# Optimization experiments

Measured on AMD Instinct MI355X. Metric: run time of the kernel, lower is better.

## Reference

```python
import jax, jax.numpy as jnp
import numpy as np

DIM_MODEL = 512
DIM_HEAD = 64


def setup_inputs() -> dict:
    key = jax.random.key(0)
    ks = jax.random.split(key, 7)
    B, S = 4, 4096
    x = jax.random.normal(ks[0], (B, S, DIM_MODEL), dtype=jnp.float32)
    mask = jnp.ones((B, 1, S), dtype=jnp.int32)
    # torch Linear init: U(-1/sqrt(fan_in), 1/sqrt(fan_in)); stored as (in, out) for x @ W
    bound = 1.0 / np.sqrt(DIM_MODEL)
    Wq = jax.random.uniform(ks[1], (DIM_MODEL, DIM_HEAD), minval=-bound, maxval=bound, dtype=jnp.float32)
    bq = jax.random.uniform(ks[2], (DIM_HEAD,), minval=-bound, maxval=bound, dtype=jnp.float32)
    Wk = jax.random.uniform(ks[3], (DIM_MODEL, DIM_HEAD), minval=-bound, maxval=bound, dtype=jnp.float32)
    bk = jax.random.uniform(ks[4], (DIM_HEAD,), minval=-bound, maxval=bound, dtype=jnp.float32)
    Wv = jax.random.uniform(ks[5], (DIM_MODEL, DIM_HEAD), minval=-bound, maxval=bound, dtype=jnp.float32)
    bv = jax.random.uniform(ks[6], (DIM_HEAD,), minval=-bound, maxval=bound, dtype=jnp.float32)
    return {"x": x, "mask": mask, "Wq": Wq, "bq": bq, "Wk": Wk, "bk": bk, "Wv": Wv, "bv": bv}


def reference(x, mask, Wq, bq, Wk, bk, Wv, bv):
    # single-head QKV projection
    q = x @ Wq + bq  # (B, S, Dh)
    k = x @ Wk + bk
    v = x @ Wv + bv
    dot_scale = jnp.sqrt(jnp.float32(DIM_HEAD))
    # explicit O(S^2) score matrix, softmax over keys
    scores = jnp.einsum("bqd,bkd->bqk", q, k) / dot_scale  # (B, S, S)
    attn = jax.nn.softmax(scores, axis=-1)
    # faithful to source: mask applied AFTER softmax with -inf fill
    attn = jnp.where(mask == 0, jnp.float32(-jnp.inf), attn)
    return jnp.einsum("bqk,bkd->bqd", attn, v)  # (B, S, Dh)
```

## Files before the change

kernel.cpp:

```cpp
#include <hip/hip_runtime.h>
#include <hip/hip_bf16.h>

typedef _Float16 half8v __attribute__((ext_vector_type(8)));
typedef _Float16 half4v __attribute__((ext_vector_type(4)));
typedef _Float16 half2v __attribute__((ext_vector_type(2)));
typedef __fp16   fp16x2 __attribute__((ext_vector_type(2)));
typedef __attribute__((ext_vector_type(4))) float floatx4;

#define LOG2E_OVER_8 0.18033688011112042f

#if __has_builtin(__builtin_amdgcn_exp2f)
#define EXP2(x) __builtin_amdgcn_exp2f(x)
#else
#define EXP2(x) exp2f(x)
#endif


__device__ __forceinline__ void gload_lds16(const void* g, void* l) {
    __builtin_amdgcn_global_load_lds(
        (const __attribute__((address_space(1))) void*)(unsigned long long)g,
        (__attribute__((address_space(3))) void*)(unsigned)(unsigned long long)l,
        16, 0, 0);
}

__global__ __launch_bounds__(256) void wtrans_k(const float* __restrict__ Wq,
                                                const float* __restrict__ Wk,
                                                const float* __restrict__ Wv,
                                                _Float16* __restrict__ Wt) {
    int idx = blockIdx.x * 256 + threadIdx.x;
    int p = idx >> 15, rem = idx & 32767;
    int k = rem >> 6;
    int n = rem & 63;
    const float* W = (p == 0) ? Wq : ((p == 1) ? Wk : Wv);
    int ctg = p * 4 + (n >> 4), m = n & 15;
    int kc = k >> 5, quad = (k >> 3) & 3, j = k & 7;
    Wt[(((ctg << 4) + kc) * 64 + (quad << 4) + m) * 8 + j] = (_Float16)W[k * 64 + n];
}

#define XS_STRIDE 536
__global__ __launch_bounds__(256) void proj_k(const float* __restrict__ x,
                                              const _Float16* __restrict__ Wt,
                                              const float* __restrict__ bq,
                                              const float* __restrict__ bk,
                                              const float* __restrict__ bv,
                                              _Float16* __restrict__ Qh,
                                              _Float16* __restrict__ Kh,
                                              _Float16* __restrict__ Vh) {
    __shared__ _Float16 xs[2][16 * XS_STRIDE];

    int tid = threadIdx.x, l = tid & 63, wv = tid >> 6;
    int m = l & 15, quad = l >> 4;
    int row0 = blockIdx.x * 32;

#pragma unroll
    for (int s = 0; s < 2; s++)
#pragma unroll
        for (int i = 0; i < 8; i++) {
            int idx = tid + i * 256;
            int row = idx >> 7, c4 = idx & 127;
            float4 v = *(const float4*)(x + (row0 + s * 16 + row) * 512 + c4 * 4);
            union { half2v h[2]; uint2 u; } cv;
            cv.h[0][0] = (_Float16)v.x; cv.h[0][1] = (_Float16)v.y;
            cv.h[1][0] = (_Float16)v.z; cv.h[1][1] = (_Float16)v.w;
            *(uint2*)(xs[s] + row * XS_STRIDE + c4 * 4) = cv.u;
        }
    __syncthreads();

    const _Float16* arow0 = xs[0] + m * XS_STRIDE + quad * 8;
    const _Float16* arow1 = xs[1] + m * XS_STRIDE + quad * 8;

    floatx4 acc[2][3];
#pragma unroll
    for (int s = 0; s < 2; s++)
#pragma unroll
        for (int i = 0; i < 3; i++) acc[s][i] = (floatx4)(0.f);

#pragma unroll 4
    for (int kc = 0; kc < 16; kc++) {
        half8v a0 = *(const half8v*)(arow0 + kc * 32);
        half8v a1 = *(const half8v*)(arow1 + kc * 32);
#pragma unroll
        for (int ct = 0; ct < 3; ct++) {
            int ctg = wv * 3 + ct;
            half8v b = *(const half8v*)(Wt + (((ctg << 4) + kc) * 64 + l) * 8);
            acc[0][ct] = __builtin_amdgcn_mfma_f32_16x16x32_f16(a0, b, acc[0][ct], 0, 0, 0);
            acc[1][ct] = __builtin_amdgcn_mfma_f32_16x16x32_f16(a1, b, acc[1][ct], 0, 0, 0);
        }
    }

#pragma unroll
    for (int s = 0; s < 2; s++) {
        int rowb = row0 + s * 16;
#pragma unroll
        for (int ct = 0; ct < 3; ct++) {
            int ctg = wv * 3 + ct;
            int col = ctg * 16 + m;
            float bias = (ctg < 4) ? bq[col] : ((ctg < 8) ? bk[col - 64] : bv[col - 128]);
            if (ctg < 8) {
                _Float16* dst = (ctg < 4) ? Qh : Kh;
                float scl = (ctg < 4) ? LOG2E_OVER_8 : 1.0f;
                int dd = (ctg & 3) * 16 + m;
                int c = dd >> 5, quadQ = (dd >> 3) & 3, j = dd & 7;
#pragma unroll
                for (int r = 0; r < 4; r++) {
                    int row = rowb + quad * 4 + r;
                    int chunk = ((row >> 4) << 1) + c;
                    dst[(chunk * 64 + quadQ * 16 + (row & 15)) * 8 + j] =
                        (_Float16)((acc[s][ct][r] + bias) * scl);
                }
            } else {
                int dt = ctg - 8;
                int t64 = rowb >> 6, ktp = (rowb >> 5) & 1, half = (rowb >> 4) & 1;
                int chunk = t64 * 8 + dt * 2 + ktp;
                union { _Float16 h[4]; unsigned long long u; } pk;
#pragma unroll
                for (int r = 0; r < 4; r++) pk.h[r] = (_Float16)(acc[s][ct][r] + bias);
                *(unsigned long long*)(Vh + (chunk * 64 + quad * 16 + m) * 8 + half * 4) = pk.u;
            }
        }
    }
}

template <int NT>
__global__ __launch_bounds__(256, 4) void attn_k(const _Float16* __restrict__ Qh,
                                                 const _Float16* __restrict__ Kh,
                                                 const _Float16* __restrict__ Vh,
                                                 const int* __restrict__ mask,
                                                 _Float16* __restrict__ Np,
                                                 float* __restrict__ Dp,
                                                 int gshift) {
    __shared__ __align__(16) uint4 stage_lds[2][1024];

    int tid = threadIdx.x, l = tid & 63, wv = tid >> 6;
    int m = l & 15, quad = l >> 4;
    int bid = blockIdx.x;
    int grp = bid & ((1 << gshift) - 1), qblk = bid >> gshift;
    int os = grp >> 2, b = grp & 3;
    int q0 = qblk * 64 + wv * 16;

    const int* maskb = mask + b * 4096 + os * (NT * 64);
    int az = 0;
#pragma unroll
    for (int i = 0; i < NT; i++) az |= (maskb[l + i * 64] == 0);
    const bool hasz = __any(az);

    int qt_g = (b * 4096 + q0) >> 4;
    half8v qf[2];
#pragma unroll
    for (int c = 0; c < 2; c++)
        qf[c] = *(const half8v*)(Qh + ((qt_g * 2 + c) * 64 + l) * 8);

    half8v ones8;
#pragma unroll
    for (int i = 0; i < 8; i++) ones8[i] = (_Float16)1.0f;

    int tb0 = (b * 64 + os * NT) * 512;
    const uint4* kh4 = (const uint4*)Kh + tb0;
    const uint4* vh4 = (const uint4*)Vh + tb0;

    floatx4 oacc[4];
#pragma unroll
    for (int dt = 0; dt < 4; dt++) oacc[dt] = (floatx4)(0.f);
    floatx4 oden = (floatx4)(0.f);

#pragma unroll
    for (int i = 0; i < 2; i++) {
        int idx = wv * 128 + i * 64 + l;
        gload_lds16(kh4 + idx, &stage_lds[0][0] + idx);
        gload_lds16(vh4 + idx, &stage_lds[0][512] + idx);
    }
    __syncthreads();

    for (int t = 0; t < NT; t++) {
        int cur = t & 1;
        if (t + 1 < NT) {
            const uint4* ksrc = kh4 + (t + 1) * 512;
            const uint4* vsrc = vh4 + (t + 1) * 512;
            uint4* kb = &stage_lds[cur ^ 1][0];
            uint4* vb = &stage_lds[cur ^ 1][512];
#pragma unroll
            for (int i = 0; i < 2; i++) {
                int idx = wv * 128 + i * 64 + l;
                gload_lds16(ksrc + idx, kb + idx);
                gload_lds16(vsrc + idx, vb + idx);
            }
        }
        const uint4* kt4 = &stage_lds[cur][0];
        const uint4* vt4 = &stage_lds[cur][512];
#pragma unroll
        for (int sp = 0; sp < 2; sp++) {
            union { uint4 u; half8v h; } kk[4];
#pragma unroll
            for (int i = 0; i < 4; i++)
                kk[i].u = kt4[(sp * 4 + i) * 64 + l];
            uint4 vv[4];
#pragma unroll
            for (int dt = 0; dt < 4; dt++)
                vv[dt] = vt4[(dt * 2 + sp) * 64 + l];
            half8v pb8;
            {
                union { fp16x2 h2[4]; half8v h8; } pu;
#pragma unroll
                for (int se = 0; se < 2; se++) {
                    floatx4 sf = (floatx4)(0.f);
                    __builtin_amdgcn_s_setprio(1);
                    sf = __builtin_amdgcn_mfma_f32_16x16x32_f16(kk[se * 2 + 0].h, qf[0], sf, 0, 0, 0);
                    sf = __builtin_amdgcn_mfma_f32_16x16x32_f16(kk[se * 2 + 1].h, qf[1], sf, 0, 0, 0);
                    __builtin_amdgcn_s_setprio(0);
                    float p0 = EXP2(sf[0]), p1 = EXP2(sf[1]);
                    float p2 = EXP2(sf[2]), p3 = EXP2(sf[3]);
                    if (hasz) {
                        int kg = t * 64 + (sp * 2 + se) * 16 + quad * 4;
                        if (maskb[kg + 0] == 0) p0 = -__builtin_inff();
                        if (maskb[kg + 1] == 0) p1 = -__builtin_inff();
                        if (maskb[kg + 2] == 0) p2 = -__builtin_inff();
                        if (maskb[kg + 3] == 0) p3 = -__builtin_inff();
                    }
                    pu.h2[se * 2 + 0] = __builtin_amdgcn_cvt_pkrtz(p0, p1);
                    pu.h2[se * 2 + 1] = __builtin_amdgcn_cvt_pkrtz(p2, p3);
                }
                pb8 = pu.h8;
            }
            __builtin_amdgcn_s_setprio(1);
            oden = __builtin_amdgcn_mfma_f32_16x16x32_f16(ones8, pb8, oden, 0, 0, 0);
#pragma unroll
            for (int dt = 0; dt < 4; dt++) {
                union { uint4 u; half8v h; } vc; vc.u = vv[dt];
                oacc[dt] = __builtin_amdgcn_mfma_f32_16x16x32_f16(vc.h, pb8, oacc[dt], 0, 0, 0);
            }
            __builtin_amdgcn_s_setprio(0);
        }
        __syncthreads();
    }

    float* Tw = (float*)&stage_lds[0][0] + wv * (16 * 68);
    int rowb = os * 16384 + b * 4096 + q0;
    if (l < 16) Dp[rowb + l] = oden[0];
#pragma unroll
    for (int dt = 0; dt < 4; dt++)
#pragma unroll
        for (int r = 0; r < 4; r++)
            Tw[m * 68 + dt * 16 + quad * 4 + r] = oacc[dt][r];
    asm volatile("s_waitcnt lgkmcnt(0)" ::: "memory");
    __builtin_amdgcn_sched_barrier(0);
#pragma unroll
    for (int g = 0; g < 4; g++) {
        int idx = g * 64 + l;
        int row = idx >> 4, c4 = (idx & 15) * 4;
        float4 v = *(const float4*)(Tw + row * 68 + c4);
        union { half4v h; unsigned long long u; } pk;
        pk.h[0] = (_Float16)v.x; pk.h[1] = (_Float16)v.y;
        pk.h[2] = (_Float16)v.z; pk.h[3] = (_Float16)v.w;
        *(unsigned long long*)(Np + (size_t)(rowb + row) * 64 + c4) = pk.u;
    }
}

__global__ __launch_bounds__(256) void combine_k(const _Float16* __restrict__ Np,
                                                 const float* __restrict__ Dp,
                                                 float* __restrict__ out,
                                                 int spl) {
    int g4 = blockIdx.x * 256 + threadIdx.x;
    int row = g4 >> 4;
    float4 nu = make_float4(0.f, 0.f, 0.f, 0.f);
    float d = 0.f;
    for (int sp = 0; sp < spl; sp++) {
        union { unsigned long long u; half4v h; } v;
        v.u = *(const unsigned long long*)(Np + ((size_t)sp << 20) + (size_t)g4 * 4);
        nu.x += (float)v.h[0]; nu.y += (float)v.h[1];
        nu.z += (float)v.h[2]; nu.w += (float)v.h[3];
        d += Dp[sp * 16384 + row];
    }
    float inv = 1.0f / d;
    ((float4*)out)[g4] = make_float4(nu.x * inv, nu.y * inv, nu.z * inv, nu.w * inv);
}

extern "C" void kernel_launch(void* const* d_in, const int* in_sizes, int n_in,
                              void* d_out, int out_size, void* d_ws, size_t ws_size,
                              hipStream_t stream) {
    const float* x  = (const float*)d_in[0];
    const int* mask = (const int*)d_in[1];
    const float* Wq = (const float*)d_in[2];
    const float* bq = (const float*)d_in[3];
    const float* Wk = (const float*)d_in[4];
    const float* bk = (const float*)d_in[5];
    const float* Wv = (const float*)d_in[6];
    const float* bv = (const float*)d_in[7];
    float* out = (float*)d_out;

    char* ws = (char*)d_ws;
    _Float16* Wt = (_Float16*)(ws);
    _Float16* Qh = (_Float16*)(ws + 0x40000);
    _Float16* Kh = (_Float16*)(ws + 0x240000);
    _Float16* Vh = (_Float16*)(ws + 0x440000);
    float*    Dp = (float*)(ws + 0x640000);
    _Float16* Np = (_Float16*)(ws + 0x740000);

    wtrans_k<<<384, 256, 0, stream>>>(Wq, Wk, Wv, Wt);
    proj_k<<<512, 256, 0, stream>>>(x, Wt, bq, bk, bv, Qh, Kh, Vh);
    attn_k<16><<<64 * 16, 256, 0, stream>>>(Qh, Kh, Vh, mask, Np, Dp, 4);
    combine_k<<<1024, 256, 0, stream>>>(Np, Dp, out, 4);
}
```

Before: 123.0 us.

## Read K/V tiles directly from global memory and double the key-split count

Drops the double-buffered global-to-LDS staging of K/V tiles in the attention kernel, so each wave reads its K/V fragments straight from global memory (through the caches). This removes the per-tile block barriers. LDS is now used only for the output transpose, and launch bounds are raised to target more waves per SIMD. The key dimension is also split into 8 partitions instead of 4, doubling the grid and halving the tiles per block, with the combine kernel merging 8 partials. The risks are redundant global/L2 traffic, since the four waves of a block all load the same K/V data, more exposed load latency without prefetch, and extra partial output to combine.

Result: slower. 140.1 us (+13.9%).

```diff
diff --git a/kernel.cpp b/kernel.cpp
--- a/kernel.cpp
+++ b/kernel.cpp
@@ -15,13 +15,6 @@
 #define EXP2(x) exp2f(x)
 #endif
 
-
-__device__ __forceinline__ void gload_lds16(const void* g, void* l) {
-    __builtin_amdgcn_global_load_lds(
-        (const __attribute__((address_space(1))) void*)(unsigned long long)g,
-        (__attribute__((address_space(3))) void*)(unsigned)(unsigned long long)l,
-        16, 0, 0);
-}
 
 __global__ __launch_bounds__(256) void wtrans_k(const float* __restrict__ Wq,
                                                 const float* __restrict__ Wk,
@@ -122,14 +115,14 @@
 }
 
 template <int NT>
-__global__ __launch_bounds__(256, 4) void attn_k(const _Float16* __restrict__ Qh,
+__global__ __launch_bounds__(256, 6) void attn_k(const _Float16* __restrict__ Qh,
                                                  const _Float16* __restrict__ Kh,
                                                  const _Float16* __restrict__ Vh,
                                                  const int* __restrict__ mask,
                                                  _Float16* __restrict__ Np,
                                                  float* __restrict__ Dp,
                                                  int gshift) {
-    __shared__ __align__(16) uint4 stage_lds[2][1024];
+    __shared__ float T[4][16 * 68];
 
     int tid = threadIdx.x, l = tid & 63, wv = tid >> 6;
     int m = l & 15, quad = l >> 4;
@@ -163,30 +156,9 @@
     for (int dt = 0; dt < 4; dt++) oacc[dt] = (floatx4)(0.f);
     floatx4 oden = (floatx4)(0.f);
 
-#pragma unroll
-    for (int i = 0; i < 2; i++) {
-        int idx = wv * 128 + i * 64 + l;
-        gload_lds16(kh4 + idx, &stage_lds[0][0] + idx);
-        gload_lds16(vh4 + idx, &stage_lds[0][512] + idx);
-    }
-    __syncthreads();
-
     for (int t = 0; t < NT; t++) {
-        int cur = t & 1;
-        if (t + 1 < NT) {
-            const uint4* ksrc = kh4 + (t + 1) * 512;
-            const uint4* vsrc = vh4 + (t + 1) * 512;
-            uint4* kb = &stage_lds[cur ^ 1][0];
-            uint4* vb = &stage_lds[cur ^ 1][512];
-#pragma unroll
-            for (int i = 0; i < 2; i++) {
-                int idx = wv * 128 + i * 64 + l;
-                gload_lds16(ksrc + idx, kb + idx);
-                gload_lds16(vsrc + idx, vb + idx);
-            }
-        }
-        const uint4* kt4 = &stage_lds[cur][0];
-        const uint4* vt4 = &stage_lds[cur][512];
+        const uint4* kt4 = kh4 + t * 512;
+        const uint4* vt4 = vh4 + t * 512;
 #pragma unroll
         for (int sp = 0; sp < 2; sp++) {
             union { uint4 u; half8v h; } kk[4];
@@ -230,10 +202,9 @@
             }
             __builtin_amdgcn_s_setprio(0);
         }
-        __syncthreads();
-    }
-
-    float* Tw = (float*)&stage_lds[0][0] + wv * (16 * 68);
+    }
+
+    float* Tw = &T[wv][0];
     int rowb = os * 16384 + b * 4096 + q0;
     if (l < 16) Dp[rowb + l] = oden[0];
 #pragma unroll
@@ -297,6 +268,6 @@
 
     wtrans_k<<<384, 256, 0, stream>>>(Wq, Wk, Wv, Wt);
     proj_k<<<512, 256, 0, stream>>>(x, Wt, bq, bk, bv, Qh, Kh, Vh);
-    attn_k<16><<<64 * 16, 256, 0, stream>>>(Qh, Kh, Vh, mask, Np, Dp, 4);
-    combine_k<<<1024, 256, 0, stream>>>(Np, Dp, out, 4);
-}
+    attn_k<8><<<64 * 32, 256, 0, stream>>>(Qh, Kh, Vh, mask, Np, Dp, 5);
+    combine_k<<<1024, 256, 0, stream>>>(Np, Dp, out, 8);
+}
```
